# Optimization experiments

Measured on AMD Instinct MI355X. Metric: run time of the kernel, lower is better.

The kernel has to match this reference:

```python
import jax, jax.numpy as jnp
import numpy as np

B, T, D = 64, 512, 1024          # batch, time_steps (== seq_len), input_dim
ACT_DIM, UOUT, OUT = 1024, 1024, 512  # hidden size, unit_output_dim, output_dim


def setup_inputs() -> dict:
    key = jax.random.key(0)
    k0, k1, k2, k3 = jax.random.split(key, 4)
    s = 0.02  # small init so the linear recurrence stays numerically tame
    return {
        "X": jax.random.normal(k0, (B, T, D), jnp.float32),
        "Wax": jax.random.normal(k1, (ACT_DIM, D), jnp.float32) * s,
        "Waa": jax.random.normal(k2, (ACT_DIM, ACT_DIM), jnp.float32) * s,
        "ba": jnp.zeros((ACT_DIM,), jnp.float32),
        "Wy": jax.random.normal(k3, (UOUT, ACT_DIM), jnp.float32) * s,
        "by": jnp.zeros((UOUT,), jnp.float32),
    }


def reference(X, Wax, Waa, ba, Wy, by):
    # Shared-weight Elman RNN cell, act = acty = Identity (module defaults).
    # Input has no NaN padding -> non_padded_length == T, every step runs the cell.
    def step(a, x_t):
        a_new = x_t @ Wax.T + a @ Waa.T + ba   # [B, ACT_DIM]
        y = a_new @ Wy.T + by                  # [B, UOUT]
        return a_new, y

    a0 = jnp.zeros((X.shape[0], Waa.shape[0]), X.dtype)
    _, Y = jax.lax.scan(step, a0, jnp.swapaxes(X, 0, 1))  # Y: [T, B, UOUT]
    Y = jnp.swapaxes(Y, 0, 1)                              # [B, T, UOUT]
    # return_sequences=False: Y[:, non_padded_length-output_dim : non_padded_length]
    return Y[:, T - OUT:T, :]
```

## Files before the change

### kernel.cpp

```cpp
#include <hip/hip_runtime.h>
#include <hip/hip_bf16.h>
#include <stdint.h>
#include <stddef.h>

using bf16 = __hip_bfloat16;
typedef short s16x8 __attribute__((ext_vector_type(8)));
typedef float f32x4 __attribute__((ext_vector_type(4)));

#define MFMA16(a, b, c) __builtin_amdgcn_mfma_f32_16x16x32_bf16((a), (b), (c), 0, 0, 0)

typedef __attribute__((address_space(1))) void gvoid;
typedef __attribute__((address_space(3))) void lvoid;
#define GLL16(gp, lp) __builtin_amdgcn_global_load_lds((gvoid*)(void*)(gp), (lvoid*)(lp), 16, 0, 0)

__device__ __forceinline__ short f2bf(float x) {
    bf16 h = __float2bfloat16(x);
    return __builtin_bit_cast(short, h);
}

__global__ void cvt_bf16(const float* __restrict__ in, bf16* __restrict__ out, int n) {
    int i = (blockIdx.x * blockDim.x + threadIdx.x) * 4;
    if (i < n) {
        float4 v = *(const float4*)(in + i);
        out[i + 0] = __float2bfloat16(v.x);
        out[i + 1] = __float2bfloat16(v.y);
        out[i + 2] = __float2bfloat16(v.z);
        out[i + 3] = __float2bfloat16(v.w);
    }
}

__global__ void zero_bf16(bf16* __restrict__ p, int n) {
    int i = (blockIdx.x * blockDim.x + threadIdx.x) * 8;
    if (i < n) {
        s16x8 z = {0, 0, 0, 0, 0, 0, 0, 0};
        *(s16x8*)(p + i) = z;
    }
}

__global__ __launch_bounds__(256) void transpose_bf16(
    const bf16* __restrict__ in, bf16* __restrict__ out)
{
    __shared__ bf16 t[64][72];
    const int bx = blockIdx.x * 64, by = blockIdx.y * 64;
    const int tid = threadIdx.x;
#pragma unroll
    for (int i = 0; i < 2; ++i) {
        const int r = (tid >> 3) + i * 32, c = (tid & 7) * 8;
        *(s16x8*)&t[r][c] = *(const s16x8*)(in + (size_t)(bx + r) * 1024 + by + c);
    }
    __syncthreads();
#pragma unroll
    for (int i = 0; i < 2; ++i) {
        const int r = (tid >> 3) + i * 32, c = (tid & 7) * 8;
        s16x8 v;
#pragma unroll
        for (int k = 0; k < 8; ++k) v[k] = __builtin_bit_cast(short, t[c + k][r]);
        *(s16x8*)(out + (size_t)(by + r) * 1024 + bx + c) = v;
    }
}

template<bool A_F32, bool OUT_F32, int REMAP>
__global__ __launch_bounds__(256) void gemm_bt(
    const void* __restrict__ Ap, const bf16* __restrict__ Bt,
    const float* __restrict__ bias, void* __restrict__ Cp)
{
    __shared__ __align__(16) bf16 lA[128 * 64];
    __shared__ __align__(16) bf16 lB[128 * 64];

    const int tid  = threadIdx.x;
    const int lane = tid & 63, wv = tid >> 6;
    const int wm = wv & 1, wn = wv >> 1;
    const int quad = lane >> 4, l16 = lane & 15;

    const int lid = blockIdx.y * 256 + blockIdx.x;
    const int wid = (lid & 7) * 256 + (lid >> 3);
    const int m0 = (wid >> 3) * 128;
    const int n0 = (wid & 7) * 128;

    const int sr = lane >> 3;
    const int sc = ((lane & 7) ^ sr) * 8;

    const int ar = tid >> 1;
    const int ah = tid & 1;

    f32x4 acc[4][4] = {};

    for (int ko = 0; ko < 1024; ko += 64) {
        if constexpr (A_F32) {
            const float* Af = (const float*)Ap;
#pragma unroll
            for (int i = 0; i < 4; ++i) {
                const int c = ah * 4 + i;
                const float* src = Af + (size_t)(m0 + ar) * 1024 + ko + c * 8;
                float4 v0 = *(const float4*)(src);
                float4 v1 = *(const float4*)(src + 4);
                s16x8 w;
                w[0] = f2bf(v0.x); w[1] = f2bf(v0.y); w[2] = f2bf(v0.z); w[3] = f2bf(v0.w);
                w[4] = f2bf(v1.x); w[5] = f2bf(v1.y); w[6] = f2bf(v1.z); w[7] = f2bf(v1.w);
                *(s16x8*)((char*)lA + ar * 128 + ((c ^ (ar & 7)) << 4)) = w;
            }
#pragma unroll
            for (int qi = 0; qi < 4; ++qi) {
                const int q = wv * 4 + qi;
                GLL16(Bt + (size_t)(n0 + q * 8 + sr) * 1024 + ko + sc, (char*)lB + q * 1024);
            }
        } else {
            const bf16* Ab = (const bf16*)Ap;
#pragma unroll
            for (int qi = 0; qi < 4; ++qi) {
                const int q = wv * 4 + qi;
                GLL16(Ab + (size_t)(m0 + q * 8 + sr) * 1024 + ko + sc, (char*)lA + q * 1024);
                GLL16(Bt + (size_t)(n0 + q * 8 + sr) * 1024 + ko + sc, (char*)lB + q * 1024);
            }
        }
        __syncthreads();
#pragma unroll
        for (int kc = 0; kc < 2; ++kc) {
            s16x8 af[4], bg[4];
#pragma unroll
            for (int mt = 0; mt < 4; ++mt) {
                const int r = 64 * wm + 16 * mt + l16;
                const int c = kc * 4 + quad;
                af[mt] = *(const s16x8*)((const char*)lA + r * 128 + ((c ^ (r & 7)) * 16));
            }
#pragma unroll
            for (int nt = 0; nt < 4; ++nt) {
                const int r = 64 * wn + 16 * nt + l16;
                const int c = kc * 4 + quad;
                bg[nt] = *(const s16x8*)((const char*)lB + r * 128 + ((c ^ (r & 7)) * 16));
            }
#pragma unroll
            for (int mt = 0; mt < 4; ++mt)
#pragma unroll
                for (int nt = 0; nt < 4; ++nt)
                    acc[mt][nt] = MFMA16(af[mt], bg[nt], acc[mt][nt]);
        }
        __syncthreads();
    }

    float bv[4];
#pragma unroll
    for (int nt = 0; nt < 4; ++nt)
        bv[nt] = bias[n0 + 64 * wn + 16 * nt + l16];

#pragma unroll
    for (int mt = 0; mt < 4; ++mt) {
#pragma unroll
        for (int r = 0; r < 4; ++r) {
            const int m = m0 + 64 * wm + 16 * mt + 4 * quad + r;
            int om = m;
            if constexpr (REMAP == 1)      om = ((m & 511) << 6) | (m >> 9);
            else if constexpr (REMAP == 2) om = ((m & 63) << 9) | (m >> 6);
#pragma unroll
            for (int nt = 0; nt < 4; ++nt) {
                const int n = n0 + 64 * wn + 16 * nt + l16;
                const float val = acc[mt][nt][r] + bv[nt];
                if constexpr (OUT_F32) ((float*)Cp)[(size_t)om * 1024 + n] = val;
                else ((bf16*)Cp)[(size_t)om * 1024 + n] = __float2bfloat16(val);
            }
        }
    }
}

__global__ __launch_bounds__(256) void powmul(
    const bf16* __restrict__ Abase, const bf16* __restrict__ Bt,
    bf16* __restrict__ Dbase)
{
    __shared__ __align__(16) bf16 lA[128 * 64];
    __shared__ __align__(16) bf16 lB[128 * 64];
    const int tid  = threadIdx.x;
    const int lane = tid & 63, wv = tid >> 6;
    const int wm = wv & 1, wn = wv >> 1;
    const int quad = lane >> 4, l16 = lane & 15;
    const int m0 = blockIdx.x * 128, n0 = blockIdx.y * 128;
    const bf16* A = Abase + (size_t)blockIdx.z * 1048576;
    bf16* D       = Dbase + (size_t)blockIdx.z * 1048576;
    const int sr = lane >> 3;
    const int sc = ((lane & 7) ^ sr) * 8;

    f32x4 acc[4][4] = {};
    for (int ko = 0; ko < 1024; ko += 64) {
#pragma unroll
        for (int qi = 0; qi < 4; ++qi) {
            const int q = wv * 4 + qi;
            GLL16(A  + (size_t)(m0 + q * 8 + sr) * 1024 + ko + sc, (char*)lA + q * 1024);
            GLL16(Bt + (size_t)(n0 + q * 8 + sr) * 1024 + ko + sc, (char*)lB + q * 1024);
        }
        __syncthreads();
#pragma unroll
        for (int kc = 0; kc < 2; ++kc) {
            s16x8 af[4], bg[4];
#pragma unroll
            for (int mt = 0; mt < 4; ++mt) {
                const int r = 64 * wm + 16 * mt + l16;
                const int c = kc * 4 + quad;
                af[mt] = *(const s16x8*)((const char*)lA + r * 128 + ((c ^ (r & 7)) * 16));
            }
#pragma unroll
            for (int nt = 0; nt < 4; ++nt) {
                const int r = 64 * wn + 16 * nt + l16;
                const int c = kc * 4 + quad;
                bg[nt] = *(const s16x8*)((const char*)lB + r * 128 + ((c ^ (r & 7)) * 16));
            }
#pragma unroll
            for (int mt = 0; mt < 4; ++mt)
#pragma unroll
                for (int nt = 0; nt < 4; ++nt)
                    acc[mt][nt] = MFMA16(af[mt], bg[nt], acc[mt][nt]);
        }
        __syncthreads();
    }
#pragma unroll
    for (int mt = 0; mt < 4; ++mt)
#pragma unroll
        for (int r = 0; r < 4; ++r) {
            const int m = m0 + 64 * wm + 16 * mt + 4 * quad + r;
#pragma unroll
            for (int nt = 0; nt < 4; ++nt) {
                const int n = n0 + 64 * wn + 16 * nt + l16;
                D[(size_t)m * 1024 + n] = __float2bfloat16(acc[mt][nt][r]);
            }
        }
}

__global__ __launch_bounds__(256) void local_step(
    const bf16* __restrict__ Bt, bf16* __restrict__ UA, int j)
{
    __shared__ __align__(16) bf16 lA[64 * 64];
    __shared__ __align__(16) bf16 lB[128 * 64];
    const int tid = threadIdx.x;
    const int lane = tid & 63, wv = tid >> 6;
    const int quad = lane >> 4, l16 = lane & 15;
    const int n0 = blockIdx.y * 128;
    const int t = blockIdx.x * 16 + j;
    const bf16* src = UA + (size_t)(t - 1) * 64 * 1024;
    bf16* dst       = UA + (size_t)t * 64 * 1024;
    const int sr = lane >> 3;
    const int sc = ((lane & 7) ^ sr) * 8;

    f32x4 acc[4][2] = {};
    for (int ko = 0; ko < 1024; ko += 64) {
#pragma unroll
        for (int qi = 0; qi < 2; ++qi) {
            const int q = wv * 2 + qi;
            GLL16(src + (size_t)(q * 8 + sr) * 1024 + ko + sc, (char*)lA + q * 1024);
        }
#pragma unroll
        for (int qi = 0; qi < 4; ++qi) {
            const int q = wv * 4 + qi;
            GLL16(Bt + (size_t)(n0 + q * 8 + sr) * 1024 + ko + sc, (char*)lB + q * 1024);
        }
        __syncthreads();
#pragma unroll
        for (int kc = 0; kc < 2; ++kc) {
            s16x8 af[4], bg[2];
#pragma unroll
            for (int mt = 0; mt < 4; ++mt) {
                const int r = 16 * mt + l16;
                const int c = kc * 4 + quad;
                af[mt] = *(const s16x8*)((const char*)lA + r * 128 + ((c ^ (r & 7)) * 16));
            }
#pragma unroll
            for (int nt = 0; nt < 2; ++nt) {
                const int r = 32 * wv + 16 * nt + l16;
                const int c = kc * 4 + quad;
                bg[nt] = *(const s16x8*)((const char*)lB + r * 128 + ((c ^ (r & 7)) * 16));
            }
#pragma unroll
            for (int mt = 0; mt < 4; ++mt)
#pragma unroll
                for (int nt = 0; nt < 2; ++nt)
                    acc[mt][nt] = MFMA16(af[mt], bg[nt], acc[mt][nt]);
        }
        __syncthreads();
    }
#pragma unroll
    for (int mt = 0; mt < 4; ++mt)
#pragma unroll
        for (int r = 0; r < 4; ++r) {
            const int b = 16 * mt + 4 * quad + r;
#pragma unroll
            for (int nt = 0; nt < 2; ++nt) {
                const int n = n0 + 32 * wv + 16 * nt + l16;
                bf16* p = dst + (size_t)b * 1024 + n;
                *p = __float2bfloat16(acc[mt][nt][r] + __bfloat162float(*p));
            }
        }
}

__global__ __launch_bounds__(64, 1) void carry_step(
    const bf16* __restrict__ P16, const bf16* __restrict__ lend,
    const bf16* __restrict__ src, bf16* __restrict__ dst)
{
    const int lane = threadIdx.x;
    const int quad = lane >> 4, l16 = lane & 15;
    const int bi = blockIdx.x & 3, nj = blockIdx.x >> 2;

    const bf16* arow = src + ((size_t)(16 * bi + l16)) * 1024;
    const bf16* wrow = P16 + ((size_t)(16 * nj + l16)) * 1024;

    const bf16* urow = lend + ((size_t)(16 * bi + 4 * quad)) * 1024 + 16 * nj + l16;
    f32x4 acc;
#pragma unroll
    for (int rr = 0; rr < 4; ++rr)
        acc[rr] = __bfloat162float(urow[(size_t)rr * 1024]);

    s16x8 av[32], wf[32];
#pragma unroll
    for (int kc = 0; kc < 32; ++kc) {
        av[kc] = *(const s16x8*)(arow + kc * 32 + quad * 8);
        wf[kc] = *(const s16x8*)(wrow + kc * 32 + quad * 8);
    }
#pragma unroll
    for (int kc = 0; kc < 32; ++kc)
        acc = MFMA16(av[kc], wf[kc], acc);

    bf16* drow = dst + ((size_t)(16 * bi + 4 * quad)) * 1024 + 16 * nj + l16;
#pragma unroll
    for (int rr = 0; rr < 4; ++rr)
        drow[(size_t)rr * 1024] = __float2bfloat16(acc[rr]);
}

__global__ __launch_bounds__(256) void fixup_k(
    const bf16* __restrict__ CIN, const bf16* __restrict__ PBase,
    bf16* __restrict__ UA)
{
    __shared__ __align__(16) bf16 lA[128 * 64];
    __shared__ __align__(16) bf16 lB[128 * 64];
    const int tid  = threadIdx.x;
    const int lane = tid & 63, wv = tid >> 6;
    const int wm = wv & 1, wn = wv >> 1;
    const int quad = lane >> 4, l16 = lane & 15;

    const int lid = blockIdx.y * 16 + blockIdx.x;
    const int wid = (lid & 7) * 16 + (lid >> 3);
    const int m0 = (wid >> 3) * 128;
    const int n0 = (wid & 7) * 128;

    const int j = blockIdx.z;
    const bf16* Bt = PBase + (size_t)j * 1048576;
    const int sr = lane >> 3;
    const int sc = ((lane & 7) ^ sr) * 8;

    f32x4 acc[4][4] = {};
    for (int ko = 0; ko < 1024; ko += 64) {
#pragma unroll
        for (int qi = 0; qi < 4; ++qi) {
            const int q = wv * 4 + qi;
            GLL16(CIN + (size_t)(m0 + q * 8 + sr) * 1024 + ko + sc, (char*)lA + q * 1024);
            GLL16(Bt  + (size_t)(n0 + q * 8 + sr) * 1024 + ko + sc, (char*)lB + q * 1024);
        }
        __syncthreads();
#pragma unroll
        for (int kc = 0; kc < 2; ++kc) {
            s16x8 af[4], bg[4];
#pragma unroll
            for (int mt = 0; mt < 4; ++mt) {
                const int r = 64 * wm + 16 * mt + l16;
                const int c = kc * 4 + quad;
                af[mt] = *(const s16x8*)((const char*)lA + r * 128 + ((c ^ (r & 7)) * 16));
            }
#pragma unroll
            for (int nt = 0; nt < 4; ++nt) {
                const int r = 64 * wn + 16 * nt + l16;
                const int c = kc * 4 + quad;
                bg[nt] = *(const s16x8*)((const char*)lB + r * 128 + ((c ^ (r & 7)) * 16));
            }
#pragma unroll
            for (int mt = 0; mt < 4; ++mt)
#pragma unroll
                for (int nt = 0; nt < 4; ++nt)
                    acc[mt][nt] = MFMA16(af[mt], bg[nt], acc[mt][nt]);
        }
        __syncthreads();
    }
#pragma unroll
    for (int mt = 0; mt < 4; ++mt)
#pragma unroll
        for (int r = 0; r < 4; ++r) {
            const int vm = m0 + 64 * wm + 16 * mt + 4 * quad + r;
            const size_t grow = (size_t)(((vm >> 6) * 16 + j) * 64 + (vm & 63));
#pragma unroll
            for (int nt = 0; nt < 4; ++nt) {
                const int n = n0 + 64 * wn + 16 * nt + l16;
                bf16* p = UA + grow * 1024 + n;
                *p = __float2bfloat16(acc[mt][nt][r] + __bfloat162float(*p));
            }
        }
}

extern "C" void kernel_launch(void* const* d_in, const int* in_sizes, int n_in,
                              void* d_out, int out_size, void* d_ws, size_t ws_size,
                              hipStream_t stream) {
    const float* X   = (const float*)d_in[0];
    const float* Wax = (const float*)d_in[1];
    const float* Waa = (const float*)d_in[2];
    const float* ba  = (const float*)d_in[3];
    const float* Wy  = (const float*)d_in[4];
    const float* by  = (const float*)d_in[5];

    char* ws = (char*)d_ws;
    bf16* UA   = (bf16*)ws;
    bf16* PB   = (bf16*)(ws + 67108864);
    bf16* Waxb = (bf16*)(ws + 100663296);
    bf16* Wyb  = (bf16*)(ws + 102760448);
    bf16* CIN  = (bf16*)(ws + 104857600);
    bf16* Tb   = CIN;
    const size_t MM = 1048576;

    const int NW = 1024 * 1024;
    cvt_bf16<<<dim3(NW / 1024), dim3(256), 0, stream>>>(Wax, Waxb, NW);
    cvt_bf16<<<dim3(NW / 1024), dim3(256), 0, stream>>>(Waa, PB,   NW);
    cvt_bf16<<<dim3(NW / 1024), dim3(256), 0, stream>>>(Wy,  Wyb,  NW);

    dim3 grid(256, 8), blk(256);
    gemm_bt<true, false, 1><<<grid, blk, 0, stream>>>(X, Waxb, ba, UA);

    transpose_bf16<<<dim3(16, 16), blk, 0, stream>>>(PB, Tb);
    powmul<<<dim3(8, 8, 1), blk, 0, stream>>>(PB, Tb, PB + 1 * MM);
    transpose_bf16<<<dim3(16, 16), blk, 0, stream>>>(PB + 1 * MM, Tb);
    powmul<<<dim3(8, 8, 2), blk, 0, stream>>>(PB, Tb, PB + 2 * MM);
    transpose_bf16<<<dim3(16, 16), blk, 0, stream>>>(PB + 3 * MM, Tb);
    powmul<<<dim3(8, 8, 4), blk, 0, stream>>>(PB, Tb, PB + 4 * MM);
    transpose_bf16<<<dim3(16, 16), blk, 0, stream>>>(PB + 7 * MM, Tb);
    powmul<<<dim3(8, 8, 8), blk, 0, stream>>>(PB, Tb, PB + 8 * MM);

    for (int j = 1; j < 16; ++j)
        local_step<<<dim3(32, 8), blk, 0, stream>>>(PB, UA, j);

    zero_bf16<<<dim3(32), dim3(256), 0, stream>>>(CIN, 65536);
    for (int c = 1; c < 32; ++c)
        carry_step<<<dim3(256), dim3(64), 0, stream>>>(
            PB + 15 * MM,
            UA  + (size_t)((c - 1) * 16 + 15) * 65536,
            CIN + (size_t)(c - 1) * 65536,
            CIN + (size_t)c * 65536);

    fixup_k<<<dim3(16, 8, 16), blk, 0, stream>>>(CIN, PB, UA);

    gemm_bt<false, true, 2><<<grid, blk, 0, stream>>>(UA, Wyb, by, (float*)d_out);
}
```

Measured before the change: 928.1 us.

## Double-buffer LDS tiles in all GEMM kernels to overlap loads with MFMA

Doubles the shared-memory A/B tiles in gemm_bt, powmul, local_step and fixup_k, so the next K-slice is prefetched with global_load_lds while MFMAs run on the current one. For the fp32 A path, the next slice is loaded into registers early and converted and written to LDS after the compute. The goal is to hide global-load latency behind compute and drop one barrier per iteration. In exchange LDS use doubles to 64KB per block, which may lower occupancy, and the fp32 path needs more registers.

```diff
diff --git a/kernel.cpp b/kernel.cpp
--- a/kernel.cpp
+++ b/kernel.cpp
@@ -64,8 +64,8 @@
     const void* __restrict__ Ap, const bf16* __restrict__ Bt,
     const float* __restrict__ bias, void* __restrict__ Cp)
 {
-    __shared__ __align__(16) bf16 lA[128 * 64];
-    __shared__ __align__(16) bf16 lB[128 * 64];
+    __shared__ __align__(16) bf16 lA[2][128 * 64];
+    __shared__ __align__(16) bf16 lB[2][128 * 64];
 
     const int tid  = threadIdx.x;
     const int lane = tid & 63, wv = tid >> 6;
@@ -79,41 +79,59 @@
 
     const int sr = lane >> 3;
     const int sc = ((lane & 7) ^ sr) * 8;
-
     const int ar = tid >> 1;
     const int ah = tid & 1;
 
+    const float* Af = (const float*)Ap;
+    const bf16*  Ab = (const bf16*)Ap;
+
     f32x4 acc[4][4] = {};
-
-    for (int ko = 0; ko < 1024; ko += 64) {
-        if constexpr (A_F32) {
-            const float* Af = (const float*)Ap;
-#pragma unroll
-            for (int i = 0; i < 4; ++i) {
-                const int c = ah * 4 + i;
-                const float* src = Af + (size_t)(m0 + ar) * 1024 + ko + c * 8;
-                float4 v0 = *(const float4*)(src);
-                float4 v1 = *(const float4*)(src + 4);
-                s16x8 w;
-                w[0] = f2bf(v0.x); w[1] = f2bf(v0.y); w[2] = f2bf(v0.z); w[3] = f2bf(v0.w);
-                w[4] = f2bf(v1.x); w[5] = f2bf(v1.y); w[6] = f2bf(v1.z); w[7] = f2bf(v1.w);
-                *(s16x8*)((char*)lA + ar * 128 + ((c ^ (ar & 7)) << 4)) = w;
-            }
-#pragma unroll
-            for (int qi = 0; qi < 4; ++qi) {
-                const int q = wv * 4 + qi;
-                GLL16(Bt + (size_t)(n0 + q * 8 + sr) * 1024 + ko + sc, (char*)lB + q * 1024);
-            }
-        } else {
-            const bf16* Ab = (const bf16*)Ap;
-#pragma unroll
-            for (int qi = 0; qi < 4; ++qi) {
-                const int q = wv * 4 + qi;
-                GLL16(Ab + (size_t)(m0 + q * 8 + sr) * 1024 + ko + sc, (char*)lA + q * 1024);
-                GLL16(Bt + (size_t)(n0 + q * 8 + sr) * 1024 + ko + sc, (char*)lB + q * 1024);
-            }
-        }
-        __syncthreads();
+    float4 vr[4][2];
+
+#define STAGE_B(buf, ko) do { \
+    _Pragma("unroll") \
+    for (int qi = 0; qi < 4; ++qi) { \
+        const int q = wv * 4 + qi; \
+        GLL16(Bt + (size_t)(n0 + q * 8 + sr) * 1024 + (ko) + sc, (char*)lB[buf] + q * 1024); \
+    } } while (0)
+#define STAGE_A_BF(buf, ko) do { \
+    _Pragma("unroll") \
+    for (int qi = 0; qi < 4; ++qi) { \
+        const int q = wv * 4 + qi; \
+        GLL16(Ab + (size_t)(m0 + q * 8 + sr) * 1024 + (ko) + sc, (char*)lA[buf] + q * 1024); \
+    } } while (0)
+#define LOAD_A_F32(ko) do { \
+    _Pragma("unroll") \
+    for (int i = 0; i < 4; ++i) { \
+        const int c = ah * 4 + i; \
+        const float* srcp = Af + (size_t)(m0 + ar) * 1024 + (ko) + c * 8; \
+        vr[i][0] = *(const float4*)(srcp); \
+        vr[i][1] = *(const float4*)(srcp + 4); \
+    } } while (0)
+#define WRITE_A_F32(buf) do { \
+    _Pragma("unroll") \
+    for (int i = 0; i < 4; ++i) { \
+        const int c = ah * 4 + i; \
+        s16x8 w; \
+        w[0] = f2bf(vr[i][0].x); w[1] = f2bf(vr[i][0].y); w[2] = f2bf(vr[i][0].z); w[3] = f2bf(vr[i][0].w); \
+        w[4] = f2bf(vr[i][1].x); w[5] = f2bf(vr[i][1].y); w[6] = f2bf(vr[i][1].z); w[7] = f2bf(vr[i][1].w); \
+        *(s16x8*)((char*)lA[buf] + ar * 128 + ((c ^ (ar & 7)) << 4)) = w; \
+    } } while (0)
+
+    if constexpr (A_F32) { LOAD_A_F32(0); WRITE_A_F32(0); }
+    else                 { STAGE_A_BF(0, 0); }
+    STAGE_B(0, 0);
+    __syncthreads();
+
+    int cur = 0;
+    for (int t = 0; t < 16; ++t) {
+        const int nxt = cur ^ 1;
+        if (t < 15) {
+            const int ko = (t + 1) * 64;
+            if constexpr (A_F32) LOAD_A_F32(ko);
+            else                 STAGE_A_BF(nxt, ko);
+            STAGE_B(nxt, ko);
+        }
 #pragma unroll
         for (int kc = 0; kc < 2; ++kc) {
             s16x8 af[4], bg[4];
@@ -121,13 +139,13 @@
             for (int mt = 0; mt < 4; ++mt) {
                 const int r = 64 * wm + 16 * mt + l16;
                 const int c = kc * 4 + quad;
-                af[mt] = *(const s16x8*)((const char*)lA + r * 128 + ((c ^ (r & 7)) * 16));
+                af[mt] = *(const s16x8*)((const char*)lA[cur] + r * 128 + ((c ^ (r & 7)) * 16));
             }
 #pragma unroll
             for (int nt = 0; nt < 4; ++nt) {
                 const int r = 64 * wn + 16 * nt + l16;
                 const int c = kc * 4 + quad;
-                bg[nt] = *(const s16x8*)((const char*)lB + r * 128 + ((c ^ (r & 7)) * 16));
+                bg[nt] = *(const s16x8*)((const char*)lB[cur] + r * 128 + ((c ^ (r & 7)) * 16));
             }
 #pragma unroll
             for (int mt = 0; mt < 4; ++mt)
@@ -135,8 +153,14 @@
                 for (int nt = 0; nt < 4; ++nt)
                     acc[mt][nt] = MFMA16(af[mt], bg[nt], acc[mt][nt]);
         }
+        if constexpr (A_F32) { if (t < 15) WRITE_A_F32(nxt); }
         __syncthreads();
-    }
+        cur = nxt;
+    }
+#undef STAGE_B
+#undef STAGE_A_BF
+#undef LOAD_A_F32
+#undef WRITE_A_F32
 
     float bv[4];
 #pragma unroll
@@ -166,8 +190,8 @@
     const bf16* __restrict__ Abase, const bf16* __restrict__ Bt,
     bf16* __restrict__ Dbase)
 {
-    __shared__ __align__(16) bf16 lA[128 * 64];
-    __shared__ __align__(16) bf16 lB[128 * 64];
+    __shared__ __align__(16) bf16 lA[2][128 * 64];
+    __shared__ __align__(16) bf16 lB[2][128 * 64];
     const int tid  = threadIdx.x;
     const int lane = tid & 63, wv = tid >> 6;
     const int wm = wv & 1, wn = wv >> 1;
@@ -178,15 +202,21 @@
     const int sr = lane >> 3;
     const int sc = ((lane & 7) ^ sr) * 8;
 
+#define STAGE_AB(buf, ko) do { \
+    _Pragma("unroll") \
+    for (int qi = 0; qi < 4; ++qi) { \
+        const int q = wv * 4 + qi; \
+        GLL16(A  + (size_t)(m0 + q * 8 + sr) * 1024 + (ko) + sc, (char*)lA[buf] + q * 1024); \
+        GLL16(Bt + (size_t)(n0 + q * 8 + sr) * 1024 + (ko) + sc, (char*)lB[buf] + q * 1024); \
+    } } while (0)
+
     f32x4 acc[4][4] = {};
-    for (int ko = 0; ko < 1024; ko += 64) {
-#pragma unroll
-        for (int qi = 0; qi < 4; ++qi) {
-            const int q = wv * 4 + qi;
-            GLL16(A  + (size_t)(m0 + q * 8 + sr) * 1024 + ko + sc, (char*)lA + q * 1024);
-            GLL16(Bt + (size_t)(n0 + q * 8 + sr) * 1024 + ko + sc, (char*)lB + q * 1024);
-        }
-        __syncthreads();
+    STAGE_AB(0, 0);
+    __syncthreads();
+    int cur = 0;
+    for (int t = 0; t < 16; ++t) {
+        const int nxt = cur ^ 1;
+        if (t < 15) STAGE_AB(nxt, (t + 1) * 64);
 #pragma unroll
         for (int kc = 0; kc < 2; ++kc) {
             s16x8 af[4], bg[4];
@@ -194,13 +224,13 @@
             for (int mt = 0; mt < 4; ++mt) {
                 const int r = 64 * wm + 16 * mt + l16;
                 const int c = kc * 4 + quad;
-                af[mt] = *(const s16x8*)((const char*)lA + r * 128 + ((c ^ (r & 7)) * 16));
+                af[mt] = *(const s16x8*)((const char*)lA[cur] + r * 128 + ((c ^ (r & 7)) * 16));
             }
 #pragma unroll
             for (int nt = 0; nt < 4; ++nt) {
                 const int r = 64 * wn + 16 * nt + l16;
                 const int c = kc * 4 + quad;
-                bg[nt] = *(const s16x8*)((const char*)lB + r * 128 + ((c ^ (r & 7)) * 16));
+                bg[nt] = *(const s16x8*)((const char*)lB[cur] + r * 128 + ((c ^ (r & 7)) * 16));
             }
 #pragma unroll
             for (int mt = 0; mt < 4; ++mt)
@@ -209,7 +239,9 @@
                     acc[mt][nt] = MFMA16(af[mt], bg[nt], acc[mt][nt]);
         }
         __syncthreads();
-    }
+        cur = nxt;
+    }
+#undef STAGE_AB
 #pragma unroll
     for (int mt = 0; mt < 4; ++mt)
 #pragma unroll
@@ -226,31 +258,37 @@
 __global__ __launch_bounds__(256) void local_step(
     const bf16* __restrict__ Bt, bf16* __restrict__ UA, int j)
 {
-    __shared__ __align__(16) bf16 lA[64 * 64];
-    __shared__ __align__(16) bf16 lB[128 * 64];
+    __shared__ __align__(16) bf16 lA[2][64 * 64];
+    __shared__ __align__(16) bf16 lB[2][128 * 64];
     const int tid = threadIdx.x;
     const int lane = tid & 63, wv = tid >> 6;
     const int quad = lane >> 4, l16 = lane & 15;
     const int n0 = blockIdx.y * 128;
-    const int t = blockIdx.x * 16 + j;
-    const bf16* src = UA + (size_t)(t - 1) * 64 * 1024;
-    bf16* dst       = UA + (size_t)t * 64 * 1024;
+    const int t_ = blockIdx.x * 16 + j;
+    const bf16* src = UA + (size_t)(t_ - 1) * 64 * 1024;
+    bf16* dst       = UA + (size_t)t_ * 64 * 1024;
     const int sr = lane >> 3;
     const int sc = ((lane & 7) ^ sr) * 8;
 
+#define STAGE_AB(buf, ko) do { \
+    _Pragma("unroll") \
+    for (int qi = 0; qi < 2; ++qi) { \
+        const int q = wv * 2 + qi; \
+        GLL16(src + (size_t)(q * 8 + sr) * 1024 + (ko) + sc, (char*)lA[buf] + q * 1024); \
+    } \
+    _Pragma("unroll") \
+    for (int qi = 0; qi < 4; ++qi) { \
+        const int q = wv * 4 + qi; \
+        GLL16(Bt + (size_t)(n0 + q * 8 + sr) * 1024 + (ko) + sc, (char*)lB[buf] + q * 1024); \
+    } } while (0)
+
     f32x4 acc[4][2] = {};
-    for (int ko = 0; ko < 1024; ko += 64) {
-#pragma unroll
-        for (int qi = 0; qi < 2; ++qi) {
-            const int q = wv * 2 + qi;
-            GLL16(src + (size_t)(q * 8 + sr) * 1024 + ko + sc, (char*)lA + q * 1024);
-        }
-#pragma unroll
-        for (int qi = 0; qi < 4; ++qi) {
-            const int q = wv * 4 + qi;
-            GLL16(Bt + (size_t)(n0 + q * 8 + sr) * 1024 + ko + sc, (char*)lB + q * 1024);
-        }
-        __syncthreads();
+    STAGE_AB(0, 0);
+    __syncthreads();
+    int cur = 0;
+    for (int t = 0; t < 16; ++t) {
+        const int nxt = cur ^ 1;
+        if (t < 15) STAGE_AB(nxt, (t + 1) * 64);
 #pragma unroll
         for (int kc = 0; kc < 2; ++kc) {
             s16x8 af[4], bg[2];
@@ -258,13 +296,13 @@
             for (int mt = 0; mt < 4; ++mt) {
                 const int r = 16 * mt + l16;
                 const int c = kc * 4 + quad;
-                af[mt] = *(const s16x8*)((const char*)lA + r * 128 + ((c ^ (r & 7)) * 16));
+                af[mt] = *(const s16x8*)((const char*)lA[cur] + r * 128 + ((c ^ (r & 7)) * 16));
             }
 #pragma unroll
             for (int nt = 0; nt < 2; ++nt) {
                 const int r = 32 * wv + 16 * nt + l16;
                 const int c = kc * 4 + quad;
-                bg[nt] = *(const s16x8*)((const char*)lB + r * 128 + ((c ^ (r & 7)) * 16));
+                bg[nt] = *(const s16x8*)((const char*)lB[cur] + r * 128 + ((c ^ (r & 7)) * 16));
             }
 #pragma unroll
             for (int mt = 0; mt < 4; ++mt)
@@ -273,7 +311,9 @@
                     acc[mt][nt] = MFMA16(af[mt], bg[nt], acc[mt][nt]);
         }
         __syncthreads();
-    }
+        cur = nxt;
+    }
+#undef STAGE_AB
 #pragma unroll
     for (int mt = 0; mt < 4; ++mt)
 #pragma unroll
@@ -325,8 +365,8 @@
     const bf16* __restrict__ CIN, const bf16* __restrict__ PBase,
     bf16* __restrict__ UA)
 {
-    __shared__ __align__(16) bf16 lA[128 * 64];
-    __shared__ __align__(16) bf16 lB[128 * 64];
+    __shared__ __align__(16) bf16 lA[2][128 * 64];
+    __shared__ __align__(16) bf16 lB[2][128 * 64];
     const int tid  = threadIdx.x;
     const int lane = tid & 63, wv = tid >> 6;
     const int wm = wv & 1, wn = wv >> 1;
@@ -342,15 +382,21 @@
     const int sr = lane >> 3;
     const int sc = ((lane & 7) ^ sr) * 8;
 
+#define STAGE_AB(buf, ko) do { \
+    _Pragma("unroll") \
+    for (int qi = 0; qi < 4; ++qi) { \
+        const int q = wv * 4 + qi; \
+        GLL16(CIN + (size_t)(m0 + q * 8 + sr) * 1024 + (ko) + sc, (char*)lA[buf] + q * 1024); \
+        GLL16(Bt  + (size_t)(n0 + q * 8 + sr) * 1024 + (ko) + sc, (char*)lB[buf] + q * 1024); \
+    } } while (0)
+
     f32x4 acc[4][4] = {};
-    for (int ko = 0; ko < 1024; ko += 64) {
-#pragma unroll
-        for (int qi = 0; qi < 4; ++qi) {
-            const int q = wv * 4 + qi;
-            GLL16(CIN + (size_t)(m0 + q * 8 + sr) * 1024 + ko + sc, (char*)lA + q * 1024);
-            GLL16(Bt  + (size_t)(n0 + q * 8 + sr) * 1024 + ko + sc, (char*)lB + q * 1024);
-        }
-        __syncthreads();
+    STAGE_AB(0, 0);
+    __syncthreads();
+    int cur = 0;
+    for (int t = 0; t < 16; ++t) {
+        const int nxt = cur ^ 1;
+        if (t < 15) STAGE_AB(nxt, (t + 1) * 64);
 #pragma unroll
         for (int kc = 0; kc < 2; ++kc) {
             s16x8 af[4], bg[4];
@@ -358,13 +404,13 @@
             for (int mt = 0; mt < 4; ++mt) {
                 const int r = 64 * wm + 16 * mt + l16;
                 const int c = kc * 4 + quad;
-                af[mt] = *(const s16x8*)((const char*)lA + r * 128 + ((c ^ (r & 7)) * 16));
+                af[mt] = *(const s16x8*)((const char*)lA[cur] + r * 128 + ((c ^ (r & 7)) * 16));
             }
 #pragma unroll
             for (int nt = 0; nt < 4; ++nt) {
                 const int r = 64 * wn + 16 * nt + l16;
                 const int c = kc * 4 + quad;
-                bg[nt] = *(const s16x8*)((const char*)lB + r * 128 + ((c ^ (r & 7)) * 16));
+                bg[nt] = *(const s16x8*)((const char*)lB[cur] + r * 128 + ((c ^ (r & 7)) * 16));
             }
 #pragma unroll
             for (int mt = 0; mt < 4; ++mt)
@@ -373,7 +419,9 @@
                     acc[mt][nt] = MFMA16(af[mt], bg[nt], acc[mt][nt]);
         }
         __syncthreads();
-    }
+        cur = nxt;
+    }
+#undef STAGE_AB
 #pragma unroll
     for (int mt = 0; mt < 4; ++mt)
 #pragma unroll
```

Measured after the change: 967.6 us. +4.3%, slower.
